# Kernel tuning notes

Hardware: AMD Instinct MI355X
Metric: run time of the kernel (lower is better)

Reference implementation:

```python
import jax, jax.numpy as jnp
import numpy as np

N_A = 100000
N_B = 100000


def _mean_agg(x_src, src, dst, n_dst):
    # gather source features along edges, mean-aggregate into destination nodes
    msgs = x_src[src]                                        # [E, d]
    s = jax.ops.segment_sum(msgs, dst, num_segments=n_dst)   # [n_dst, d]
    ones = jnp.ones((dst.shape[0], 1), dtype=x_src.dtype)
    cnt = jax.ops.segment_sum(ones, dst, num_segments=n_dst)
    return s / jnp.maximum(cnt, jnp.asarray(1.0, x_src.dtype))


def setup_inputs() -> dict:
    key = jax.random.key(0)
    ks = jax.random.split(key, 13)
    E = 1200000
    d = 64
    return {
        "x_A": jax.random.normal(ks[0], (N_A, d), jnp.float32),
        "x_B": jax.random.normal(ks[1], (N_B, d), jnp.float32),
        "Wn": jax.random.normal(ks[2], (2, 3, d, d), jnp.float32) * 0.1,
        "Wr": jax.random.normal(ks[3], (2, 3, d, d), jnp.float32) * 0.1,
        "b": jax.random.normal(ks[4], (2, 3, d), jnp.float32) * 0.1,
        "W_out": jax.random.normal(ks[5], (d, d), jnp.float32) * 0.1,
        "b_out": jax.random.normal(ks[6], (d,), jnp.float32) * 0.1,
        "src0": jax.random.randint(ks[7], (E,), 0, N_A, jnp.int64 if jax.config.jax_enable_x64 else jnp.int32),
        "dst0": jax.random.randint(ks[8], (E,), 0, N_B, jnp.int32),
        "src1": jax.random.randint(ks[9], (E,), 0, N_B, jnp.int32),
        "dst1": jax.random.randint(ks[10], (E,), 0, N_A, jnp.int32),
        "src2": jax.random.randint(ks[11], (E,), 0, N_A, jnp.int32),
        "dst2": jax.random.randint(ks[12], (E,), 0, N_A, jnp.int32),
    }


def reference(x_A, x_B, Wn, Wr, b, W_out, b_out,
              src0, dst0, src1, dst1, src2, dst2):
    # Two stacked heterogeneous conv layers (SAGEConv-style per edge type,
    # summed across edge types per destination node type), then Linear+ReLU head.
    for l in range(2):
        m0 = _mean_agg(x_A, src0, dst0, N_B)  # A -> B
        m1 = _mean_agg(x_B, src1, dst1, N_A)  # B -> A
        m2 = _mean_agg(x_A, src2, dst2, N_A)  # A -> A
        new_B = m0 @ Wn[l, 0] + x_B @ Wr[l, 0] + b[l, 0]
        new_A = (m1 @ Wn[l, 1] + x_A @ Wr[l, 1] + b[l, 1]
                 + m2 @ Wn[l, 2] + x_A @ Wr[l, 2] + b[l, 2])
        x_A, x_B = new_A, new_B
    out_A = jax.nn.relu(x_A @ W_out + b_out)
    out_B = jax.nn.relu(x_B @ W_out + b_out)
    return jnp.concatenate([out_A, out_B], axis=0)  # [N_A + N_B, d]
```

## Files before the change

### kernel.cpp

```cpp
#include <hip/hip_runtime.h>
#include <hip/hip_bf16.h>

typedef __bf16 bf16_t;
typedef unsigned short u16;
typedef short short8 __attribute__((ext_vector_type(8)));
typedef float f32x4 __attribute__((ext_vector_type(4)));

#define BSHIFT 9
#define CAP 8192
#define PTILE 8192

__device__ inline short f2bs(float v) {
    bf16_t h = (bf16_t)v;
    return __builtin_bit_cast(short, h);
}
__device__ inline float uif(unsigned u) { return __builtin_bit_cast(float, u); }

__global__ __launch_bounds__(1024, 8) void mega_prep_partition(
    const float* __restrict__ xA, const float* __restrict__ xB,
    const float* __restrict__ Wn, const float* __restrict__ Wr,
    const float* __restrict__ Wout, const float* __restrict__ b,
    const float* __restrict__ b_out,
    const int* __restrict__ s0, const int* __restrict__ d0,
    const int* __restrict__ s1, const int* __restrict__ d1,
    const int* __restrict__ s2, const int* __restrict__ d2,
    u16* __restrict__ plane0, u16* __restrict__ wh,
    int* __restrict__ gcursor, float* __restrict__ biasC,
    int* __restrict__ pairs,
    int NA, int NB, int E, int total, int ntiles) {
    __shared__ __align__(16) char smem[32768];
    int bi = blockIdx.x;
    int tid = threadIdx.x;

    if (bi < ntiles) {
        int* hist = (int*)smem;
        int* gbase = hist + 1024;
        hist[tid] = 0;
        __syncthreads();
        int tile = bi * PTILE;
        int mybkt[8], mypk[8], myrank[8];
#pragma unroll
        for (int j = 0; j < 8; j++) {
            int idx = tile + j * 1024 + tid;
            int g = -1, s = 0;
            if (idx < total) {
                if (idx < E) { s = s0[idx]; g = d0[idx]; }
                else if (idx < 2 * E) { s = s1[idx - E]; g = NB + d1[idx - E]; }
                else { s = s2[idx - 2 * E]; g = NB + NA + d2[idx - 2 * E]; }
            }
            if (g >= 0) {
                mybkt[j] = g >> BSHIFT;
                mypk[j] = ((g & ((1 << BSHIFT) - 1)) << 17) | s;
                myrank[j] = atomicAdd(&hist[mybkt[j]], 1);
            } else mybkt[j] = -1;
        }
        __syncthreads();
        {
            int c = hist[tid];
            if (c) gbase[tid] = tid * CAP + atomicAdd(&gcursor[tid], c);
        }
        __syncthreads();
#pragma unroll
        for (int j = 0; j < 8; j++) {
            if (mybkt[j] >= 0)
                pairs[gbase[mybkt[j]] + myrank[j]] = mypk[j];
        }
        return;
    }

    bi -= ntiles;
    int nA4 = NA * 16, nB4 = NB * 16;
    int bA = (nA4 + 1023) / 1024, bB = (nB4 + 1023) / 1024;
    if (bi < bA + bB) {
        const float* in = (bi < bA) ? xA : xB;
        u16* out = (bi < bA) ? plane0 : plane0 + (size_t)NA * 64;
        int i = (bi < bA ? bi : bi - bA) * 1024 + tid;
        int n4 = (bi < bA) ? nA4 : nB4;
        if (i >= n4) return;
        float4 v = ((const float4*)in)[i];
        u16 o[4];
        o[0] = (u16)f2bs(v.x); o[1] = (u16)f2bs(v.y);
        o[2] = (u16)f2bs(v.z); o[3] = (u16)f2bs(v.w);
        *(uint2*)(out + (size_t)i * 4) = *(uint2*)o;
        return;
    }
    if (bi < bA + bB + 11) {
        int mat = bi - bA - bB;
        u16* dstp = wh + (size_t)mat * 4096;
        for (int i = tid; i < 4096; i += 1024) {
            int k = i >> 6, n = i & 63;
            float v;
            if (mat < 6) v = Wn[(size_t)mat * 4096 + i];
            else if (mat < 8) v = Wr[(size_t)((mat - 6) * 3 + 0) * 4096 + i];
            else if (mat < 10) v = Wr[(size_t)((mat - 8) * 3 + 1) * 4096 + i]
                                 + Wr[(size_t)((mat - 8) * 3 + 2) * 4096 + i];
            else v = Wout[i];
            dstp[n * 64 + k] = (u16)f2bs(v);
        }
        return;
    }
    if (bi < bA + bB + 11 + 5) {
        int c = bi - bA - bB - 11;
        const float* Wsrc;
        const float* Wsrc2 = nullptr;
        if (c == 0) Wsrc = Wn + (size_t)3 * 4096;
        else if (c == 1) Wsrc = Wr + (size_t)3 * 4096;
        else if (c == 2) Wsrc = Wn + (size_t)4 * 4096;
        else if (c == 3) Wsrc = Wn + (size_t)5 * 4096;
        else { Wsrc = Wr + (size_t)4 * 4096; Wsrc2 = Wr + (size_t)5 * 4096; }
        float* Ws = (float*)smem;
        float* Wo = Ws + 4096;
        for (int i = tid; i < 4096; i += 1024) {
            float w = Wsrc[i];
            if (Wsrc2) w += Wsrc2[i];
            Ws[i] = w;
            Wo[i] = Wout[i];
        }
        __syncthreads();
        u16* dstp = wh + (size_t)(11 + c) * 4096;
        for (int it = 0; it < 4; ++it) {
            int i = it * 1024 + tid;
            int k = i >> 6, n = i & 63;
            float p0 = 0.f, p1 = 0.f, p2 = 0.f, p3 = 0.f;
#pragma unroll
            for (int j = 0; j < 64; j += 4) {
                p0 += Ws[k * 64 + j]     * Wo[j * 64 + n];
                p1 += Ws[k * 64 + j + 1] * Wo[(j + 1) * 64 + n];
                p2 += Ws[k * 64 + j + 2] * Wo[(j + 2) * 64 + n];
                p3 += Ws[k * 64 + j + 3] * Wo[(j + 3) * 64 + n];
            }
            dstp[n * 64 + k] = (u16)f2bs((p0 + p1) + (p2 + p3));
        }
        return;
    }
    if (tid < 64) {
        int n = tid;
        float s0v = b_out[n], s1v = b_out[n];
        for (int j = 0; j < 64; j++) {
            float wo = Wout[j * 64 + n];
            s0v += b[3 * 64 + j] * wo;
            s1v += (b[4 * 64 + j] + b[5 * 64 + j]) * wo;
        }
        biasC[0 * 64 + n] = b[0 * 64 + n];
        biasC[1 * 64 + n] = b[1 * 64 + n] + b[2 * 64 + n];
        biasC[2 * 64 + n] = s0v;
        biasC[3 * 64 + n] = s1v;
    }
}

__global__ __launch_bounds__(512) void bucket_fill(const int* __restrict__ pairs,
                                                   const int* __restrict__ gcursor,
                                                   int* __restrict__ off_s,
                                                   int* __restrict__ off_e,
                                                   int* __restrict__ colidx, int M) {
    int b = blockIdx.x;
    int gb = b << BSHIFT;
    __shared__ int cnt[512], cur[512], wsum[8];
    int tid = threadIdx.x;
    int lane = tid & 63, w = tid >> 6;
    int p0 = b * CAP, p1 = p0 + gcursor[b];
    cnt[tid] = 0;
    __syncthreads();
    for (int e = p0 + tid; e < p1; e += 512)
        atomicAdd(&cnt[(unsigned)pairs[e] >> 17], 1);
    __syncthreads();
    int v = cnt[tid];
    int x = v;
#pragma unroll
    for (int off = 1; off < 64; off <<= 1) {
        int n = __shfl_up(x, off);
        if (lane >= off) x += n;
    }
    if (lane == 63) wsum[w] = x;
    __syncthreads();
    if (tid == 0) {
        int s = 0;
#pragma unroll
        for (int i = 0; i < 8; i++) { int t = wsum[i]; wsum[i] = s; s += t; }
    }
    __syncthreads();
    int excl = x - v + wsum[w];
    cur[tid] = excl;
    int g = gb + tid;
    if (g < M) { off_s[g] = p0 + excl; off_e[g] = p0 + excl + v; }
    __syncthreads();
    for (int e = p0 + tid; e < p1; e += 512) {
        int p = pairs[e];
        int pos = atomicAdd(&cur[(unsigned)p >> 17], 1);
        colidx[p0 + pos] = p & 0x1FFFF;
    }
}

__device__ __forceinline__ void acc8(uint4 u, f32x4& a0, f32x4& a1) {
    a0[0] += uif(u.x << 16); a0[1] += uif(u.x & 0xFFFF0000u);
    a0[2] += uif(u.y << 16); a0[3] += uif(u.y & 0xFFFF0000u);
    a1[0] += uif(u.z << 16); a1[1] += uif(u.z & 0xFFFF0000u);
    a1[2] += uif(u.w << 16); a1[3] += uif(u.w & 0xFFFF0000u);
}

__device__ __forceinline__ uint4 gather_seg(const char* __restrict__ tab,
                                            const int* __restrict__ colidx,
                                            int s0, int s1, unsigned fo) {
    f32x4 a0 = {0.f, 0.f, 0.f, 0.f}, a1 = {0.f, 0.f, 0.f, 0.f};
    int e = s0;
    if (e + 3 < s1) {
        int c0 = colidx[e], c1 = colidx[e + 1];
        int c2 = colidx[e + 2], c3 = colidx[e + 3];
        while (e + 7 < s1) {
            uint4 u0 = *(const uint4*)(tab + (((unsigned)c0 << 7) | fo));
            uint4 u1 = *(const uint4*)(tab + (((unsigned)c1 << 7) | fo));
            uint4 u2 = *(const uint4*)(tab + (((unsigned)c2 << 7) | fo));
            uint4 u3 = *(const uint4*)(tab + (((unsigned)c3 << 7) | fo));
            c0 = colidx[e + 4]; c1 = colidx[e + 5];
            c2 = colidx[e + 6]; c3 = colidx[e + 7];
            acc8(u0, a0, a1); acc8(u1, a0, a1);
            acc8(u2, a0, a1); acc8(u3, a0, a1);
            e += 4;
        }
        {
            uint4 u0 = *(const uint4*)(tab + (((unsigned)c0 << 7) | fo));
            uint4 u1 = *(const uint4*)(tab + (((unsigned)c1 << 7) | fo));
            uint4 u2 = *(const uint4*)(tab + (((unsigned)c2 << 7) | fo));
            uint4 u3 = *(const uint4*)(tab + (((unsigned)c3 << 7) | fo));
            acc8(u0, a0, a1); acc8(u1, a0, a1);
            acc8(u2, a0, a1); acc8(u3, a0, a1);
            e += 4;
        }
    }
    for (; e < s1; ++e) {
        int c = colidx[e];
        uint4 u = *(const uint4*)(tab + (((unsigned)c << 7) | fo));
        acc8(u, a0, a1);
    }
    float inv = 1.0f / fmaxf((float)(s1 - s0), 1.0f);
    u16 o[8];
#pragma unroll
    for (int i = 0; i < 4; i++) o[i] = (u16)f2bs(a0[i] * inv);
#pragma unroll
    for (int i = 0; i < 4; i++) o[4 + i] = (u16)f2bs(a1[i] * inv);
    return *(uint4*)o;
}

template <int L2>
__global__ __launch_bounds__(256) void fused_layer(
    const u16* __restrict__ plane_in, void* __restrict__ outv,
    const int* __restrict__ colidx,
    const int* __restrict__ off_s, const int* __restrict__ off_e,
    const u16* __restrict__ wh, const float* __restrict__ biasC,
    int NA, int NB, int blocksBf) {
    __shared__ __align__(16) u16 mS[32][72];
    const int tid = threadIdx.x;
    const int w = tid >> 6, lane = tid & 63;
    const int oct = lane >> 3, fl = lane & 7;
    const unsigned fo = (unsigned)(fl << 4);
    const char* pA = (const char*)plane_in;
    const char* pB = (const char*)(plane_in + (size_t)NA * 64);
    const int r = lane & 15, q = lane >> 4;
    short8 zf;
#pragma unroll
    for (int j = 0; j < 8; j++) zf[j] = 0;

    if ((int)blockIdx.x < blocksBf) {
        const int row0 = blockIdx.x * 32;
        const int rt = w >> 1;
        const int tbase = (w & 1) * 2;
        const int arow = row0 + rt * 16 + r;
        const bool av = arow < NB;
        short8 ax0 = av ? *(const short8*)(pB + (size_t)arow * 128 + q * 16) : zf;
        short8 ax1 = av ? *(const short8*)(pB + (size_t)arow * 128 + 64 + q * 16) : zf;
        {
            int seg = w * 8 + oct;
            int brow = row0 + seg;
            int s0 = 0, s1 = 0;
            if (brow < NB) { s0 = off_s[brow]; s1 = off_e[brow]; }
            uint4 mv = gather_seg(pA, colidx, s0, s1, fo);
            *(uint4*)&mS[seg][fl * 8] = mv;
        }
        __syncthreads();
        const u16* WmT = wh + (size_t)(L2 ? 11 : 0) * 4096;
        const u16* WxT = wh + (size_t)(L2 ? 12 : 6) * 4096;
        const float* bb = biasC + (size_t)(L2 ? 2 : 0) * 64;
        f32x4 acc[2];
#pragma unroll
        for (int t2 = 0; t2 < 2; t2++) {
            float bv = bb[(tbase + t2) * 16 + r];
            acc[t2][0] = bv; acc[t2][1] = bv; acc[t2][2] = bv; acc[t2][3] = bv;
        }
#pragma unroll
        for (int ks = 0; ks < 2; ks++) {
            short8 am = *(const short8*)&mS[rt * 16 + r][ks * 32 + q * 8];
            short8 ax = ks ? ax1 : ax0;
#pragma unroll
            for (int t2 = 0; t2 < 2; t2++) {
                size_t widx = (size_t)((tbase + t2) * 16 + r) * 64 + ks * 32 + q * 8;
                acc[t2] = __builtin_amdgcn_mfma_f32_16x16x32_bf16(am, *(const short8*)(WmT + widx), acc[t2], 0, 0, 0);
                acc[t2] = __builtin_amdgcn_mfma_f32_16x16x32_bf16(ax, *(const short8*)(WxT + widx), acc[t2], 0, 0, 0);
            }
        }
#pragma unroll
        for (int t2 = 0; t2 < 2; t2++) {
            int col = (tbase + t2) * 16 + r;
#pragma unroll
            for (int rr = 0; rr < 4; rr++) {
                int row = row0 + rt * 16 + q * 4 + rr;
                if (row < NB) {
                    float v = acc[t2][rr];
                    if (L2) __builtin_nontemporal_store(fmaxf(v, 0.0f),
                                (float*)outv + (size_t)(NA + row) * 64 + col);
                    else ((u16*)outv)[(size_t)(NA + row) * 64 + col] = (u16)f2bs(v);
                }
            }
        }
    } else {
        const int row0 = ((int)blockIdx.x - blocksBf) * 16;
        const int t = w;
        const int arow = row0 + r;
        const bool av = arow < NA;
        short8 ax0 = av ? *(const short8*)(pA + (size_t)arow * 128 + q * 16) : zf;
        short8 ax1 = av ? *(const short8*)(pA + (size_t)arow * 128 + 64 + q * 16) : zf;
        {
            int seg = w * 8 + oct;
            int rrow = row0 + (seg & 15);
            bool m2 = seg >= 16;
            int s0 = 0, s1 = 0;
            if (rrow < NA) {
                int g = m2 ? (NB + NA + rrow) : (NB + rrow);
                s0 = off_s[g]; s1 = off_e[g];
            }
            uint4 mv = gather_seg(m2 ? pA : pB, colidx, s0, s1, fo);
            *(uint4*)&mS[seg][fl * 8] = mv;
        }
        __syncthreads();
        const u16* Wm1T = wh + (size_t)(L2 ? 13 : 1) * 4096;
        const u16* Wm2T = wh + (size_t)(L2 ? 14 : 2) * 4096;
        const u16* WxT  = wh + (size_t)(L2 ? 15 : 8) * 4096;
        const float* bb = biasC + (size_t)(L2 ? 3 : 1) * 64;
        f32x4 acc;
        {
            float bv = bb[t * 16 + r];
            acc[0] = bv; acc[1] = bv; acc[2] = bv; acc[3] = bv;
        }
#pragma unroll
        for (int ks = 0; ks < 2; ks++) {
            short8 am1 = *(const short8*)&mS[r][ks * 32 + q * 8];
            short8 am2 = *(const short8*)&mS[16 + r][ks * 32 + q * 8];
            short8 ax = ks ? ax1 : ax0;
            size_t widx = (size_t)(t * 16 + r) * 64 + ks * 32 + q * 8;
            acc = __builtin_amdgcn_mfma_f32_16x16x32_bf16(am1, *(const short8*)(Wm1T + widx), acc, 0, 0, 0);
            acc = __builtin_amdgcn_mfma_f32_16x16x32_bf16(am2, *(const short8*)(Wm2T + widx), acc, 0, 0, 0);
            acc = __builtin_amdgcn_mfma_f32_16x16x32_bf16(ax, *(const short8*)(WxT + widx), acc, 0, 0, 0);
        }
        {
            int col = t * 16 + r;
#pragma unroll
            for (int rr = 0; rr < 4; rr++) {
                int row = row0 + q * 4 + rr;
                if (row < NA) {
                    float v = acc[rr];
                    if (L2) __builtin_nontemporal_store(fmaxf(v, 0.0f),
                                (float*)outv + (size_t)row * 64 + col);
                    else ((u16*)outv)[(size_t)row * 64 + col] = (u16)f2bs(v);
                }
            }
        }
    }
}

extern "C" void kernel_launch(void* const* d_in, const int* in_sizes, int n_in,
                              void* d_out, int out_size, void* d_ws, size_t ws_size,
                              hipStream_t stream) {
    const float* xA_in = (const float*)d_in[0];
    const float* xB_in = (const float*)d_in[1];
    const float* Wn = (const float*)d_in[2];
    const float* Wr = (const float*)d_in[3];
    const float* b = (const float*)d_in[4];
    const float* W_out = (const float*)d_in[5];
    const float* b_out = (const float*)d_in[6];
    const int* src0 = (const int*)d_in[7];
    const int* dst0 = (const int*)d_in[8];
    const int* src1 = (const int*)d_in[9];
    const int* dst1 = (const int*)d_in[10];
    const int* src2 = (const int*)d_in[11];
    const int* dst2 = (const int*)d_in[12];

    const int NA = in_sizes[0] / 64;
    const int NB = in_sizes[1] / 64;
    const int E = in_sizes[7];
    const int M = NB + NA + NA;
    const int total = 3 * E;
    const int K = (M + (1 << BSHIFT) - 1) >> BSHIFT;

    const size_t PL = (size_t)(NA + NB) * 64;
    u16* plane[2];
    plane[0] = (u16*)d_ws;
    plane[1] = plane[0] + PL;
    u16* wh     = plane[1] + PL;
    int* gcursor= (int*)(wh + 16 * 4096);
    float* biasC= (float*)(gcursor + 1024);
    int* off_s  = (int*)(biasC + 256);
    int* off_e  = off_s + M;
    int* colidx = off_e + M;
    int* pairs  = colidx + (size_t)K * CAP;

    int bA = (NA * 16 + 1023) / 1024, bB = (NB * 16 + 1023) / 1024;
    int ntiles = (total + PTILE - 1) / PTILE;
    hipMemsetAsync(gcursor, 0, 1024 * 4, stream);
    mega_prep_partition<<<ntiles + bA + bB + 11 + 5 + 1, 1024, 0, stream>>>(
        xA_in, xB_in, Wn, Wr, W_out, b, b_out,
        src0, dst0, src1, dst1, src2, dst2,
        plane[0], wh, gcursor, biasC, pairs, NA, NB, E, total, ntiles);

    bucket_fill<<<K, 512, 0, stream>>>(pairs, gcursor, off_s, off_e, colidx, M);

    const int blocksBf = (NB + 31) / 32;
    const int blocksAf = (NA + 15) / 16;
    fused_layer<0><<<blocksBf + blocksAf, 256, 0, stream>>>(
        plane[0], plane[1], colidx, off_s, off_e, wh, biasC, NA, NB, blocksBf);
    fused_layer<1><<<blocksBf + blocksAf, 256, 0, stream>>>(
        plane[1], d_out, colidx, off_s, off_e, wh, biasC, NA, NB, blocksBf);
}
```

Before: 359.8 us.

## Make each wave own a full 16-row tile in fused layer kernels

Reorganizes fused_layer so each 64-lane wave handles an entire 16-row tile on its own: it gathers all segments for its rows into a private LDS slice and computes all four 16-column output tiles with MFMA. Blocks shrink to 128 threads (two independent waves), and the block-wide __syncthreads is replaced by a wave barrier. The aim is to remove cross-wave synchronization stalls, where uneven gather lengths made every wave wait for the slowest one, and to let waves progress independently. In exchange each wave does serial gathers over twice as many segments (two passes per lane), holds more accumulators in registers, and reloads the weights per wave.

```diff
diff --git a/kernel.cpp b/kernel.cpp
--- a/kernel.cpp
+++ b/kernel.cpp
@@ -242,69 +242,72 @@
 }
 
 template <int L2>
-__global__ __launch_bounds__(256) void fused_layer(
+__global__ __launch_bounds__(128) void fused_layer(
     const u16* __restrict__ plane_in, void* __restrict__ outv,
     const int* __restrict__ colidx,
     const int* __restrict__ off_s, const int* __restrict__ off_e,
     const u16* __restrict__ wh, const float* __restrict__ biasC,
-    int NA, int NB, int blocksBf) {
-    __shared__ __align__(16) u16 mS[32][72];
+    int NA, int NB, int tileB) {
+    __shared__ __align__(16) u16 mS[2][2][16][72];
     const int tid = threadIdx.x;
     const int w = tid >> 6, lane = tid & 63;
     const int oct = lane >> 3, fl = lane & 7;
     const unsigned fo = (unsigned)(fl << 4);
+    const int r = lane & 15, q = lane >> 4;
+    const int tileA = (NA + 15) / 16;
+    const int wv = (int)blockIdx.x * 2 + w;
+    if (wv >= tileB + tileA) return;
     const char* pA = (const char*)plane_in;
     const char* pB = (const char*)(plane_in + (size_t)NA * 64);
-    const int r = lane & 15, q = lane >> 4;
+    u16 (* __restrict__ mT0)[72] = mS[w][0];
+    u16 (* __restrict__ mT1)[72] = mS[w][1];
     short8 zf;
 #pragma unroll
     for (int j = 0; j < 8; j++) zf[j] = 0;
 
-    if ((int)blockIdx.x < blocksBf) {
-        const int row0 = blockIdx.x * 32;
-        const int rt = w >> 1;
-        const int tbase = (w & 1) * 2;
-        const int arow = row0 + rt * 16 + r;
+    if (wv < tileB) {
+        const int row0 = wv * 16;
+        const int arow = row0 + r;
         const bool av = arow < NB;
         short8 ax0 = av ? *(const short8*)(pB + (size_t)arow * 128 + q * 16) : zf;
         short8 ax1 = av ? *(const short8*)(pB + (size_t)arow * 128 + 64 + q * 16) : zf;
-        {
-            int seg = w * 8 + oct;
-            int brow = row0 + seg;
+#pragma unroll
+        for (int s = 0; s < 2; s++) {
+            int row = row0 + oct + s * 8;
             int s0 = 0, s1 = 0;
-            if (brow < NB) { s0 = off_s[brow]; s1 = off_e[brow]; }
+            if (row < NB) { s0 = off_s[row]; s1 = off_e[row]; }
             uint4 mv = gather_seg(pA, colidx, s0, s1, fo);
-            *(uint4*)&mS[seg][fl * 8] = mv;
-        }
-        __syncthreads();
+            *(uint4*)&mT0[oct + s * 8][fl * 8] = mv;
+        }
+        __builtin_amdgcn_wave_barrier();
         const u16* WmT = wh + (size_t)(L2 ? 11 : 0) * 4096;
         const u16* WxT = wh + (size_t)(L2 ? 12 : 6) * 4096;
         const float* bb = biasC + (size_t)(L2 ? 2 : 0) * 64;
-        f32x4 acc[2];
-#pragma unroll
-        for (int t2 = 0; t2 < 2; t2++) {
-            float bv = bb[(tbase + t2) * 16 + r];
-            acc[t2][0] = bv; acc[t2][1] = bv; acc[t2][2] = bv; acc[t2][3] = bv;
+        f32x4 acc[4];
+#pragma unroll
+        for (int t = 0; t < 4; t++) {
+            float bv = bb[t * 16 + r];
+            acc[t][0] = bv; acc[t][1] = bv; acc[t][2] = bv; acc[t][3] = bv;
         }
 #pragma unroll
         for (int ks = 0; ks < 2; ks++) {
-            short8 am = *(const short8*)&mS[rt * 16 + r][ks * 32 + q * 8];
+            short8 am = *(const short8*)&mT0[r][ks * 32 + q * 8];
             short8 ax = ks ? ax1 : ax0;
 #pragma unroll
-            for (int t2 = 0; t2 < 2; t2++) {
-                size_t widx = (size_t)((tbase + t2) * 16 + r) * 64 + ks * 32 + q * 8;
-                acc[t2] = __builtin_amdgcn_mfma_f32_16x16x32_bf16(am, *(const short8*)(WmT + widx), acc[t2], 0, 0, 0);
-                acc[t2] = __builtin_amdgcn_mfma_f32_16x16x32_bf16(ax, *(const short8*)(WxT + widx), acc[t2], 0, 0, 0);
-            }
-        }
-#pragma unroll
-        for (int t2 = 0; t2 < 2; t2++) {
-            int col = (tbase + t2) * 16 + r;
+            for (int t = 0; t < 4; t++) {
+                size_t widx = (size_t)(t * 16 + r) * 64 + ks * 32 + q * 8;
+                acc[t] = __builtin_amdgcn_mfma_f32_16x16x32_bf16(am, *(const short8*)(WmT + widx), acc[t], 0, 0, 0);
+                acc[t] = __builtin_amdgcn_mfma_f32_16x16x32_bf16(ax, *(const short8*)(WxT + widx), acc[t], 0, 0, 0);
+            }
+        }
+#pragma unroll
+        for (int t = 0; t < 4; t++) {
+            int col = t * 16 + r;
 #pragma unroll
             for (int rr = 0; rr < 4; rr++) {
-                int row = row0 + rt * 16 + q * 4 + rr;
+                int row = row0 + q * 4 + rr;
                 if (row < NB) {
-                    float v = acc[t2][rr];
+                    float v = acc[t][rr];
                     if (L2) __builtin_nontemporal_store(fmaxf(v, 0.0f),
                                 (float*)outv + (size_t)(NA + row) * 64 + col);
                     else ((u16*)outv)[(size_t)(NA + row) * 64 + col] = (u16)f2bs(v);
@@ -312,51 +315,57 @@
             }
         }
     } else {
-        const int row0 = ((int)blockIdx.x - blocksBf) * 16;
-        const int t = w;
+        const int row0 = (wv - tileB) * 16;
         const int arow = row0 + r;
         const bool av = arow < NA;
         short8 ax0 = av ? *(const short8*)(pA + (size_t)arow * 128 + q * 16) : zf;
         short8 ax1 = av ? *(const short8*)(pA + (size_t)arow * 128 + 64 + q * 16) : zf;
-        {
-            int seg = w * 8 + oct;
-            int rrow = row0 + (seg & 15);
-            bool m2 = seg >= 16;
-            int s0 = 0, s1 = 0;
-            if (rrow < NA) {
-                int g = m2 ? (NB + NA + rrow) : (NB + rrow);
-                s0 = off_s[g]; s1 = off_e[g];
-            }
-            uint4 mv = gather_seg(m2 ? pA : pB, colidx, s0, s1, fo);
-            *(uint4*)&mS[seg][fl * 8] = mv;
-        }
-        __syncthreads();
+#pragma unroll
+        for (int s = 0; s < 2; s++) {
+            int row = row0 + oct + s * 8;
+            int a0 = 0, a1 = 0, b0 = 0, b1 = 0;
+            if (row < NA) {
+                int g1 = NB + row, g2 = NB + NA + row;
+                a0 = off_s[g1]; a1 = off_e[g1];
+                b0 = off_s[g2]; b1 = off_e[g2];
+            }
+            uint4 v1 = gather_seg(pB, colidx, a0, a1, fo);
+            *(uint4*)&mT0[oct + s * 8][fl * 8] = v1;
+            uint4 v2 = gather_seg(pA, colidx, b0, b1, fo);
+            *(uint4*)&mT1[oct + s * 8][fl * 8] = v2;
+        }
+        __builtin_amdgcn_wave_barrier();
         const u16* Wm1T = wh + (size_t)(L2 ? 13 : 1) * 4096;
         const u16* Wm2T = wh + (size_t)(L2 ? 14 : 2) * 4096;
         const u16* WxT  = wh + (size_t)(L2 ? 15 : 8) * 4096;
         const float* bb = biasC + (size_t)(L2 ? 3 : 1) * 64;
-        f32x4 acc;
-        {
+        f32x4 acc[4];
+#pragma unroll
+        for (int t = 0; t < 4; t++) {
             float bv = bb[t * 16 + r];
-            acc[0] = bv; acc[1] = bv; acc[2] = bv; acc[3] = bv;
+            acc[t][0] = bv; acc[t][1] = bv; acc[t][2] = bv; acc[t][3] = bv;
         }
 #pragma unroll
         for (int ks = 0; ks < 2; ks++) {
-            short8 am1 = *(const short8*)&mS[r][ks * 32 + q * 8];
-            short8 am2 = *(const short8*)&mS[16 + r][ks * 32 + q * 8];
+            short8 am1 = *(const short8*)&mT0[r][ks * 32 + q * 8];
+            short8 am2 = *(const short8*)&mT1[r][ks * 32 + q * 8];
             short8 ax = ks ? ax1 : ax0;
-            size_t widx = (size_t)(t * 16 + r) * 64 + ks * 32 + q * 8;
-            acc = __builtin_amdgcn_mfma_f32_16x16x32_bf16(am1, *(const short8*)(Wm1T + widx), acc, 0, 0, 0);
-            acc = __builtin_amdgcn_mfma_f32_16x16x32_bf16(am2, *(const short8*)(Wm2T + widx), acc, 0, 0, 0);
-            acc = __builtin_amdgcn_mfma_f32_16x16x32_bf16(ax, *(const short8*)(WxT + widx), acc, 0, 0, 0);
-        }
-        {
+#pragma unroll
+            for (int t = 0; t < 4; t++) {
+                size_t widx = (size_t)(t * 16 + r) * 64 + ks * 32 + q * 8;
+                acc[t] = __builtin_amdgcn_mfma_f32_16x16x32_bf16(am1, *(const short8*)(Wm1T + widx), acc[t], 0, 0, 0);
+                acc[t] = __builtin_amdgcn_mfma_f32_16x16x32_bf16(am2, *(const short8*)(Wm2T + widx), acc[t], 0, 0, 0);
+                acc[t] = __builtin_amdgcn_mfma_f32_16x16x32_bf16(ax, *(const short8*)(WxT + widx), acc[t], 0, 0, 0);
+            }
+        }
+#pragma unroll
+        for (int t = 0; t < 4; t++) {
             int col = t * 16 + r;
 #pragma unroll
             for (int rr = 0; rr < 4; rr++) {
                 int row = row0 + q * 4 + rr;
                 if (row < NA) {
-                    float v = acc[rr];
+                    float v = acc[t][rr];
                     if (L2) __builtin_nontemporal_store(fmaxf(v, 0.0f),
                                 (float*)outv + (size_t)row * 64 + col);
                     else ((u16*)outv)[(size_t)row * 64 + col] = (u16)f2bs(v);
@@ -412,10 +421,11 @@
 
     bucket_fill<<<K, 512, 0, stream>>>(pairs, gcursor, off_s, off_e, colidx, M);
 
-    const int blocksBf = (NB + 31) / 32;
-    const int blocksAf = (NA + 15) / 16;
-    fused_layer<0><<<blocksBf + blocksAf, 256, 0, stream>>>(
-        plane[0], plane[1], colidx, off_s, off_e, wh, biasC, NA, NB, blocksBf);
-    fused_layer<1><<<blocksBf + blocksAf, 256, 0, stream>>>(
-        plane[1], d_out, colidx, off_s, off_e, wh, biasC, NA, NB, blocksBf);
-}
+    const int tileB = (NB + 15) / 16;
+    const int tileA = (NA + 15) / 16;
+    const int nblk = (tileB + tileA + 1) / 2;
+    fused_layer<0><<<nblk, 128, 0, stream>>>(
+        plane[0], plane[1], colidx, off_s, off_e, wh, biasC, NA, NB, tileB);
+    fused_layer<1><<<nblk, 128, 0, stream>>>(
+        plane[1], d_out, colidx, off_s, off_e, wh, biasC, NA, NB, tileB);
+}
```

Result: slower. 370.9 us (+3.1%).

## Gather two segments per 8-lane group and double rows per block

Applied to the files above, without the earlier changes.

Each 8-lane group now interleaves the gathers for two destination segments (two B rows, or the m1 and m2 segments of one A row), which keeps more independent loads in flight per thread. Block tiles double to 64 B rows and 32 A rows, so each block computes more output tiles per weight load and the grid has half as many blocks. The cost is higher register use for the dual accumulators, predicated loads in the unified loop, and fewer blocks for load balancing across skewed degrees.

```diff
diff --git a/kernel.cpp b/kernel.cpp
--- a/kernel.cpp
+++ b/kernel.cpp
@@ -198,47 +198,39 @@
     a1[2] += uif(u.w << 16); a1[3] += uif(u.w & 0xFFFF0000u);
 }
 
-__device__ __forceinline__ uint4 gather_seg(const char* __restrict__ tab,
-                                            const int* __restrict__ colidx,
-                                            int s0, int s1, unsigned fo) {
-    f32x4 a0 = {0.f, 0.f, 0.f, 0.f}, a1 = {0.f, 0.f, 0.f, 0.f};
-    int e = s0;
-    if (e + 3 < s1) {
-        int c0 = colidx[e], c1 = colidx[e + 1];
-        int c2 = colidx[e + 2], c3 = colidx[e + 3];
-        while (e + 7 < s1) {
-            uint4 u0 = *(const uint4*)(tab + (((unsigned)c0 << 7) | fo));
-            uint4 u1 = *(const uint4*)(tab + (((unsigned)c1 << 7) | fo));
-            uint4 u2 = *(const uint4*)(tab + (((unsigned)c2 << 7) | fo));
-            uint4 u3 = *(const uint4*)(tab + (((unsigned)c3 << 7) | fo));
-            c0 = colidx[e + 4]; c1 = colidx[e + 5];
-            c2 = colidx[e + 6]; c3 = colidx[e + 7];
-            acc8(u0, a0, a1); acc8(u1, a0, a1);
-            acc8(u2, a0, a1); acc8(u3, a0, a1);
-            e += 4;
-        }
-        {
-            uint4 u0 = *(const uint4*)(tab + (((unsigned)c0 << 7) | fo));
-            uint4 u1 = *(const uint4*)(tab + (((unsigned)c1 << 7) | fo));
-            uint4 u2 = *(const uint4*)(tab + (((unsigned)c2 << 7) | fo));
-            uint4 u3 = *(const uint4*)(tab + (((unsigned)c3 << 7) | fo));
-            acc8(u0, a0, a1); acc8(u1, a0, a1);
-            acc8(u2, a0, a1); acc8(u3, a0, a1);
-            e += 4;
-        }
-    }
-    for (; e < s1; ++e) {
-        int c = colidx[e];
-        uint4 u = *(const uint4*)(tab + (((unsigned)c << 7) | fo));
-        acc8(u, a0, a1);
-    }
-    float inv = 1.0f / fmaxf((float)(s1 - s0), 1.0f);
-    u16 o[8];
-#pragma unroll
-    for (int i = 0; i < 4; i++) o[i] = (u16)f2bs(a0[i] * inv);
-#pragma unroll
-    for (int i = 0; i < 4; i++) o[4 + i] = (u16)f2bs(a1[i] * inv);
-    return *(uint4*)o;
+__device__ __forceinline__ void gather2(const char* __restrict__ ta, int a0, int a1,
+                                        const char* __restrict__ tb, int b0, int b1,
+                                        const int* __restrict__ colidx, unsigned fo,
+                                        u16* __restrict__ outA, u16* __restrict__ outB) {
+    f32x4 pa0 = {0.f,0.f,0.f,0.f}, pa1 = {0.f,0.f,0.f,0.f};
+    f32x4 qb0 = {0.f,0.f,0.f,0.f}, qb1 = {0.f,0.f,0.f,0.f};
+    int e1 = a0, e2 = b0;
+    while (e1 < a1 || e2 < b1) {
+        int n1 = a1 - e1; n1 = n1 > 4 ? 4 : n1;
+        int n2 = b1 - e2; n2 = n2 > 4 ? 4 : n2;
+        uint4 r1[4], r2[4];
+#pragma unroll
+        for (int j = 0; j < 4; j++)
+            if (j < n1) { int c = colidx[e1 + j]; r1[j] = *(const uint4*)(ta + (((unsigned)c << 7) | fo)); }
+#pragma unroll
+        for (int j = 0; j < 4; j++)
+            if (j < n2) { int c = colidx[e2 + j]; r2[j] = *(const uint4*)(tb + (((unsigned)c << 7) | fo)); }
+#pragma unroll
+        for (int j = 0; j < 4; j++) if (j < n1) acc8(r1[j], pa0, pa1);
+#pragma unroll
+        for (int j = 0; j < 4; j++) if (j < n2) acc8(r2[j], qb0, qb1);
+        e1 += n1; e2 += n2;
+    }
+    float inva = 1.0f / fmaxf((float)(a1 - a0), 1.0f);
+    float invb = 1.0f / fmaxf((float)(b1 - b0), 1.0f);
+    u16 oa[8], ob[8];
+#pragma unroll
+    for (int i = 0; i < 4; i++) {
+        oa[i] = (u16)f2bs(pa0[i] * inva); oa[4 + i] = (u16)f2bs(pa1[i] * inva);
+        ob[i] = (u16)f2bs(qb0[i] * invb); ob[4 + i] = (u16)f2bs(qb1[i] * invb);
+    }
+    *(uint4*)outA = *(uint4*)oa;
+    *(uint4*)outB = *(uint4*)ob;
 }
 
 template <int L2>
@@ -248,7 +240,7 @@
     const int* __restrict__ off_s, const int* __restrict__ off_e,
     const u16* __restrict__ wh, const float* __restrict__ biasC,
     int NA, int NB, int blocksBf) {
-    __shared__ __align__(16) u16 mS[32][72];
+    __shared__ __align__(16) u16 mS[64][72];
     const int tid = threadIdx.x;
     const int w = tid >> 6, lane = tid & 63;
     const int oct = lane >> 3, fl = lane & 7;
@@ -256,55 +248,54 @@
     const char* pA = (const char*)plane_in;
     const char* pB = (const char*)(plane_in + (size_t)NA * 64);
     const int r = lane & 15, q = lane >> 4;
+    const int seg = w * 8 + oct;
     short8 zf;
 #pragma unroll
     for (int j = 0; j < 8; j++) zf[j] = 0;
 
     if ((int)blockIdx.x < blocksBf) {
-        const int row0 = blockIdx.x * 32;
-        const int rt = w >> 1;
-        const int tbase = (w & 1) * 2;
-        const int arow = row0 + rt * 16 + r;
+        const int row0 = blockIdx.x * 64;
+        const int arow = row0 + w * 16 + r;
         const bool av = arow < NB;
         short8 ax0 = av ? *(const short8*)(pB + (size_t)arow * 128 + q * 16) : zf;
         short8 ax1 = av ? *(const short8*)(pB + (size_t)arow * 128 + 64 + q * 16) : zf;
         {
-            int seg = w * 8 + oct;
-            int brow = row0 + seg;
-            int s0 = 0, s1 = 0;
-            if (brow < NB) { s0 = off_s[brow]; s1 = off_e[brow]; }
-            uint4 mv = gather_seg(pA, colidx, s0, s1, fo);
-            *(uint4*)&mS[seg][fl * 8] = mv;
+            int ra = row0 + seg, rb = row0 + seg + 32;
+            int a0 = 0, a1 = 0, b0 = 0, b1 = 0;
+            if (ra < NB) { a0 = off_s[ra]; a1 = off_e[ra]; }
+            if (rb < NB) { b0 = off_s[rb]; b1 = off_e[rb]; }
+            gather2(pA, a0, a1, pA, b0, b1, colidx, fo,
+                    &mS[seg][fl * 8], &mS[seg + 32][fl * 8]);
         }
         __syncthreads();
         const u16* WmT = wh + (size_t)(L2 ? 11 : 0) * 4096;
         const u16* WxT = wh + (size_t)(L2 ? 12 : 6) * 4096;
         const float* bb = biasC + (size_t)(L2 ? 2 : 0) * 64;
-        f32x4 acc[2];
-#pragma unroll
-        for (int t2 = 0; t2 < 2; t2++) {
-            float bv = bb[(tbase + t2) * 16 + r];
-            acc[t2][0] = bv; acc[t2][1] = bv; acc[t2][2] = bv; acc[t2][3] = bv;
+        f32x4 acc[4];
+#pragma unroll
+        for (int t = 0; t < 4; t++) {
+            float bv = bb[t * 16 + r];
+            acc[t][0] = bv; acc[t][1] = bv; acc[t][2] = bv; acc[t][3] = bv;
         }
 #pragma unroll
         for (int ks = 0; ks < 2; ks++) {
-            short8 am = *(const short8*)&mS[rt * 16 + r][ks * 32 + q * 8];
+            short8 am = *(const short8*)&mS[w * 16 + r][ks * 32 + q * 8];
             short8 ax = ks ? ax1 : ax0;
 #pragma unroll
-            for (int t2 = 0; t2 < 2; t2++) {
-                size_t widx = (size_t)((tbase + t2) * 16 + r) * 64 + ks * 32 + q * 8;
-                acc[t2] = __builtin_amdgcn_mfma_f32_16x16x32_bf16(am, *(const short8*)(WmT + widx), acc[t2], 0, 0, 0);
-                acc[t2] = __builtin_amdgcn_mfma_f32_16x16x32_bf16(ax, *(const short8*)(WxT + widx), acc[t2], 0, 0, 0);
-            }
-        }
-#pragma unroll
-        for (int t2 = 0; t2 < 2; t2++) {
-            int col = (tbase + t2) * 16 + r;
+            for (int t = 0; t < 4; t++) {
+                size_t widx = (size_t)(t * 16 + r) * 64 + ks * 32 + q * 8;
+                acc[t] = __builtin_amdgcn_mfma_f32_16x16x32_bf16(am, *(const short8*)(WmT + widx), acc[t], 0, 0, 0);
+                acc[t] = __builtin_amdgcn_mfma_f32_16x16x32_bf16(ax, *(const short8*)(WxT + widx), acc[t], 0, 0, 0);
+            }
+        }
+#pragma unroll
+        for (int t = 0; t < 4; t++) {
+            int col = t * 16 + r;
 #pragma unroll
             for (int rr = 0; rr < 4; rr++) {
-                int row = row0 + rt * 16 + q * 4 + rr;
+                int row = row0 + w * 16 + q * 4 + rr;
                 if (row < NB) {
-                    float v = acc[t2][rr];
+                    float v = acc[t][rr];
                     if (L2) __builtin_nontemporal_store(fmaxf(v, 0.0f),
                                 (float*)outv + (size_t)(NA + row) * 64 + col);
                     else ((u16*)outv)[(size_t)(NA + row) * 64 + col] = (u16)f2bs(v);
@@ -312,51 +303,56 @@
             }
         }
     } else {
-        const int row0 = ((int)blockIdx.x - blocksBf) * 16;
-        const int t = w;
-        const int arow = row0 + r;
+        const int row0 = ((int)blockIdx.x - blocksBf) * 32;
+        const int rt = w >> 1;
+        const int tbase = (w & 1) * 2;
+        const int arow = row0 + rt * 16 + r;
         const bool av = arow < NA;
         short8 ax0 = av ? *(const short8*)(pA + (size_t)arow * 128 + q * 16) : zf;
         short8 ax1 = av ? *(const short8*)(pA + (size_t)arow * 128 + 64 + q * 16) : zf;
         {
-            int seg = w * 8 + oct;
-            int rrow = row0 + (seg & 15);
-            bool m2 = seg >= 16;
-            int s0 = 0, s1 = 0;
-            if (rrow < NA) {
-                int g = m2 ? (NB + NA + rrow) : (NB + rrow);
-                s0 = off_s[g]; s1 = off_e[g];
-            }
-            uint4 mv = gather_seg(m2 ? pA : pB, colidx, s0, s1, fo);
-            *(uint4*)&mS[seg][fl * 8] = mv;
+            int row = row0 + seg;
+            int a0 = 0, a1 = 0, b0 = 0, b1 = 0;
+            if (row < NA) {
+                int g1 = NB + row, g2 = NB + NA + row;
+                a0 = off_s[g1]; a1 = off_e[g1];
+                b0 = off_s[g2]; b1 = off_e[g2];
+            }
+            gather2(pB, a0, a1, pA, b0, b1, colidx, fo,
+                    &mS[seg][fl * 8], &mS[seg + 32][fl * 8]);
         }
         __syncthreads();
         const u16* Wm1T = wh + (size_t)(L2 ? 13 : 1) * 4096;
         const u16* Wm2T = wh + (size_t)(L2 ? 14 : 2) * 4096;
         const u16* WxT  = wh + (size_t)(L2 ? 15 : 8) * 4096;
         const float* bb = biasC + (size_t)(L2 ? 3 : 1) * 64;
-        f32x4 acc;
-        {
-            float bv = bb[t * 16 + r];
-            acc[0] = bv; acc[1] = bv; acc[2] = bv; acc[3] = bv;
+        f32x4 acc[2];
+#pragma unroll
+        for (int t2 = 0; t2 < 2; t2++) {
+            float bv = bb[(tbase + t2) * 16 + r];
+            acc[t2][0] = bv; acc[t2][1] = bv; acc[t2][2] = bv; acc[t2][3] = bv;
         }
 #pragma unroll
         for (int ks = 0; ks < 2; ks++) {
-            short8 am1 = *(const short8*)&mS[r][ks * 32 + q * 8];
-            short8 am2 = *(const short8*)&mS[16 + r][ks * 32 + q * 8];
+            short8 am1 = *(const short8*)&mS[rt * 16 + r][ks * 32 + q * 8];
+            short8 am2 = *(const short8*)&mS[32 + rt * 16 + r][ks * 32 + q * 8];
             short8 ax = ks ? ax1 : ax0;
-            size_t widx = (size_t)(t * 16 + r) * 64 + ks * 32 + q * 8;
-            acc = __builtin_amdgcn_mfma_f32_16x16x32_bf16(am1, *(const short8*)(Wm1T + widx), acc, 0, 0, 0);
-            acc = __builtin_amdgcn_mfma_f32_16x16x32_bf16(am2, *(const short8*)(Wm2T + widx), acc, 0, 0, 0);
-            acc = __builtin_amdgcn_mfma_f32_16x16x32_bf16(ax, *(const short8*)(WxT + widx), acc, 0, 0, 0);
-        }
-        {
-            int col = t * 16 + r;
+#pragma unroll
+            for (int t2 = 0; t2 < 2; t2++) {
+                size_t widx = (size_t)((tbase + t2) * 16 + r) * 64 + ks * 32 + q * 8;
+                acc[t2] = __builtin_amdgcn_mfma_f32_16x16x32_bf16(am1, *(const short8*)(Wm1T + widx), acc[t2], 0, 0, 0);
+                acc[t2] = __builtin_amdgcn_mfma_f32_16x16x32_bf16(am2, *(const short8*)(Wm2T + widx), acc[t2], 0, 0, 0);
+                acc[t2] = __builtin_amdgcn_mfma_f32_16x16x32_bf16(ax, *(const short8*)(WxT + widx), acc[t2], 0, 0, 0);
+            }
+        }
+#pragma unroll
+        for (int t2 = 0; t2 < 2; t2++) {
+            int col = (tbase + t2) * 16 + r;
 #pragma unroll
             for (int rr = 0; rr < 4; rr++) {
-                int row = row0 + q * 4 + rr;
+                int row = row0 + rt * 16 + q * 4 + rr;
                 if (row < NA) {
-                    float v = acc[rr];
+                    float v = acc[t2][rr];
                     if (L2) __builtin_nontemporal_store(fmaxf(v, 0.0f),
                                 (float*)outv + (size_t)row * 64 + col);
                     else ((u16*)outv)[(size_t)row * 64 + col] = (u16)f2bs(v);
@@ -412,8 +408,8 @@
 
     bucket_fill<<<K, 512, 0, stream>>>(pairs, gcursor, off_s, off_e, colidx, M);
 
-    const int blocksBf = (NB + 31) / 32;
-    const int blocksAf = (NA + 15) / 16;
+    const int blocksBf = (NB + 63) / 64;
+    const int blocksAf = (NA + 31) / 32;
     fused_layer<0><<<blocksBf + blocksAf, 256, 0, stream>>>(
         plane[0], plane[1], colidx, off_s, off_e, wh, biasC, NA, NB, blocksBf);
     fused_layer<1><<<blocksBf + blocksAf, 256, 0, stream>>>(
```

After: 442.2 us. +22.9%, slower.

## Sort destination rows by degree to balance gather work per block

Applied to the files above, without the earlier changes.

Adds a degree histogram kernel and a counting-sort scatter kernel that build per-node-type row permutations grouped by in-degree (capped at 127). Both fused layers then process rows in permuted order, indirecting the input feature load, segment offsets and output writes through the permutation. The intent is to cut load imbalance and lane divergence in the per-segment gather loops, since each 8-lane group waits on the longest segment in its block. In exchange it adds two small kernel launches and an extra indirection, and output stores and self-feature loads become scattered rather than contiguous.

```diff
diff --git a/kernel.cpp b/kernel.cpp
--- a/kernel.cpp
+++ b/kernel.cpp
@@ -188,6 +188,88 @@
         int p = pairs[e];
         int pos = atomicAdd(&cur[(unsigned)p >> 17], 1);
         colidx[p0 + pos] = p & 0x1FFFF;
+    }
+}
+
+__global__ __launch_bounds__(256) void deg_hist(const int* __restrict__ off_s,
+                                                const int* __restrict__ off_e,
+                                                int* __restrict__ binsB,
+                                                int* __restrict__ binsA,
+                                                int NA, int NB) {
+    __shared__ int hB[128], hA[128];
+    int tid = threadIdx.x;
+    if (tid < 128) { hB[tid] = 0; hA[tid] = 0; }
+    __syncthreads();
+    int totalR = NB + NA;
+    for (int i = blockIdx.x * 256 + tid; i < totalR; i += gridDim.x * 256) {
+        if (i < NB) {
+            int d = off_e[i] - off_s[i];
+            atomicAdd(&hB[d > 127 ? 127 : d], 1);
+        } else {
+            int row = i - NB;
+            int d1 = off_e[NB + row] - off_s[NB + row];
+            int d2 = off_e[NB + NA + row] - off_s[NB + NA + row];
+            int d = d1 > d2 ? d1 : d2;
+            atomicAdd(&hA[d > 127 ? 127 : d], 1);
+        }
+    }
+    __syncthreads();
+    if (tid < 128) {
+        if (hB[tid]) atomicAdd(&binsB[tid], hB[tid]);
+        if (hA[tid]) atomicAdd(&binsA[tid], hA[tid]);
+    }
+}
+
+__global__ __launch_bounds__(1024) void perm_scatter(const int* __restrict__ off_s,
+                                                     const int* __restrict__ off_e,
+                                                     const int* __restrict__ binsB,
+                                                     const int* __restrict__ binsA,
+                                                     int* __restrict__ bcurB,
+                                                     int* __restrict__ bcurA,
+                                                     int* __restrict__ rowpermB,
+                                                     int* __restrict__ rowpermA,
+                                                     int NA, int NB) {
+    __shared__ int lhB[128], lhA[128], lbB[128], lbA[128], pB[128], pA[128];
+    int tid = threadIdx.x;
+    if (tid < 128) { lhB[tid] = 0; lhA[tid] = 0; }
+    __syncthreads();
+    int i = blockIdx.x * 1024 + tid;
+    int bin = -1, rank = 0, isB = 0, row = 0;
+    if (i < NB + NA) {
+        if (i < NB) {
+            row = i;
+            int d = off_e[i] - off_s[i];
+            bin = d > 127 ? 127 : d; isB = 1;
+            rank = atomicAdd(&lhB[bin], 1);
+        } else {
+            row = i - NB;
+            int d1 = off_e[NB + row] - off_s[NB + row];
+            int d2 = off_e[NB + NA + row] - off_s[NB + NA + row];
+            int d = d1 > d2 ? d1 : d2;
+            bin = d > 127 ? 127 : d;
+            rank = atomicAdd(&lhA[bin], 1);
+        }
+    }
+    __syncthreads();
+    if (tid == 0) {
+        int s = 0;
+        for (int k = 0; k < 128; k++) { pB[k] = s; s += binsB[k]; }
+        s = 0;
+        for (int k = 0; k < 128; k++) { pA[k] = s; s += binsA[k]; }
+    }
+    __syncthreads();
+    if (tid < 128) {
+        int c = lhB[tid];
+        if (c) lbB[tid] = pB[tid] + atomicAdd(&bcurB[tid], c);
+    } else if (tid < 256) {
+        int t = tid - 128;
+        int c = lhA[t];
+        if (c) lbA[t] = pA[t] + atomicAdd(&bcurA[t], c);
+    }
+    __syncthreads();
+    if (bin >= 0) {
+        if (isB) rowpermB[lbB[bin] + rank] = row;
+        else     rowpermA[lbA[bin] + rank] = row;
     }
 }
 
@@ -246,6 +328,7 @@
     const u16* __restrict__ plane_in, void* __restrict__ outv,
     const int* __restrict__ colidx,
     const int* __restrict__ off_s, const int* __restrict__ off_e,
+    const int* __restrict__ rowpermB, const int* __restrict__ rowpermA,
     const u16* __restrict__ wh, const float* __restrict__ biasC,
     int NA, int NB, int blocksBf) {
     __shared__ __align__(16) u16 mS[32][72];
@@ -264,15 +347,16 @@
         const int row0 = blockIdx.x * 32;
         const int rt = w >> 1;
         const int tbase = (w & 1) * 2;
-        const int arow = row0 + rt * 16 + r;
-        const bool av = arow < NB;
+        const int aidx = row0 + rt * 16 + r;
+        const bool av = aidx < NB;
+        const int arow = av ? rowpermB[aidx] : 0;
         short8 ax0 = av ? *(const short8*)(pB + (size_t)arow * 128 + q * 16) : zf;
         short8 ax1 = av ? *(const short8*)(pB + (size_t)arow * 128 + 64 + q * 16) : zf;
         {
             int seg = w * 8 + oct;
-            int brow = row0 + seg;
+            int idx = row0 + seg;
             int s0 = 0, s1 = 0;
-            if (brow < NB) { s0 = off_s[brow]; s1 = off_e[brow]; }
+            if (idx < NB) { int brow = rowpermB[idx]; s0 = off_s[brow]; s1 = off_e[brow]; }
             uint4 mv = gather_seg(pA, colidx, s0, s1, fo);
             *(uint4*)&mS[seg][fl * 8] = mv;
         }
@@ -302,29 +386,32 @@
             int col = (tbase + t2) * 16 + r;
 #pragma unroll
             for (int rr = 0; rr < 4; rr++) {
-                int row = row0 + rt * 16 + q * 4 + rr;
-                if (row < NB) {
+                int oidx = row0 + rt * 16 + q * 4 + rr;
+                if (oidx < NB) {
+                    int orow = rowpermB[oidx];
                     float v = acc[t2][rr];
                     if (L2) __builtin_nontemporal_store(fmaxf(v, 0.0f),
-                                (float*)outv + (size_t)(NA + row) * 64 + col);
-                    else ((u16*)outv)[(size_t)(NA + row) * 64 + col] = (u16)f2bs(v);
+                                (float*)outv + (size_t)(NA + orow) * 64 + col);
+                    else ((u16*)outv)[(size_t)(NA + orow) * 64 + col] = (u16)f2bs(v);
                 }
             }
         }
     } else {
         const int row0 = ((int)blockIdx.x - blocksBf) * 16;
         const int t = w;
-        const int arow = row0 + r;
-        const bool av = arow < NA;
+        const int aidx = row0 + r;
+        const bool av = aidx < NA;
+        const int arow = av ? rowpermA[aidx] : 0;
         short8 ax0 = av ? *(const short8*)(pA + (size_t)arow * 128 + q * 16) : zf;
         short8 ax1 = av ? *(const short8*)(pA + (size_t)arow * 128 + 64 + q * 16) : zf;
         {
             int seg = w * 8 + oct;
-            int rrow = row0 + (seg & 15);
+            int idx = row0 + (seg & 15);
             bool m2 = seg >= 16;
             int s0 = 0, s1 = 0;
-            if (rrow < NA) {
-                int g = m2 ? (NB + NA + rrow) : (NB + rrow);
+            if (idx < NA) {
+                int prow = rowpermA[idx];
+                int g = m2 ? (NB + NA + prow) : (NB + prow);
                 s0 = off_s[g]; s1 = off_e[g];
             }
             uint4 mv = gather_seg(m2 ? pA : pB, colidx, s0, s1, fo);
@@ -354,12 +441,13 @@
             int col = t * 16 + r;
 #pragma unroll
             for (int rr = 0; rr < 4; rr++) {
-                int row = row0 + q * 4 + rr;
-                if (row < NA) {
+                int oidx = row0 + q * 4 + rr;
+                if (oidx < NA) {
+                    int orow = rowpermA[oidx];
                     float v = acc[rr];
                     if (L2) __builtin_nontemporal_store(fmaxf(v, 0.0f),
-                                (float*)outv + (size_t)row * 64 + col);
-                    else ((u16*)outv)[(size_t)row * 64 + col] = (u16)f2bs(v);
+                                (float*)outv + (size_t)orow * 64 + col);
+                    else ((u16*)outv)[(size_t)orow * 64 + col] = (u16)f2bs(v);
                 }
             }
         }
@@ -394,17 +482,23 @@
     u16* plane[2];
     plane[0] = (u16*)d_ws;
     plane[1] = plane[0] + PL;
-    u16* wh     = plane[1] + PL;
-    int* gcursor= (int*)(wh + 16 * 4096);
-    float* biasC= (float*)(gcursor + 1024);
-    int* off_s  = (int*)(biasC + 256);
-    int* off_e  = off_s + M;
-    int* colidx = off_e + M;
-    int* pairs  = colidx + (size_t)K * CAP;
+    u16* wh      = plane[1] + PL;
+    int* gcursor = (int*)(wh + 16 * 4096);
+    int* binsB   = gcursor + 1024;
+    int* binsA   = binsB + 128;
+    int* bcurB   = binsA + 128;
+    int* bcurA   = bcurB + 128;
+    float* biasC = (float*)(bcurA + 128);
+    int* off_s   = (int*)(biasC + 256);
+    int* off_e   = off_s + M;
+    int* rowpermB= off_e + M;
+    int* rowpermA= rowpermB + NB;
+    int* colidx  = rowpermA + NA;
+    int* pairs   = colidx + (size_t)K * CAP;
 
     int bA = (NA * 16 + 1023) / 1024, bB = (NB * 16 + 1023) / 1024;
     int ntiles = (total + PTILE - 1) / PTILE;
-    hipMemsetAsync(gcursor, 0, 1024 * 4, stream);
+    hipMemsetAsync(gcursor, 0, (1024 + 512) * 4, stream);
     mega_prep_partition<<<ntiles + bA + bB + 11 + 5 + 1, 1024, 0, stream>>>(
         xA_in, xB_in, Wn, Wr, W_out, b, b_out,
         src0, dst0, src1, dst1, src2, dst2,
@@ -412,10 +506,16 @@
 
     bucket_fill<<<K, 512, 0, stream>>>(pairs, gcursor, off_s, off_e, colidx, M);
 
+    deg_hist<<<512, 256, 0, stream>>>(off_s, off_e, binsB, binsA, NA, NB);
+    perm_scatter<<<(NB + NA + 1023) / 1024, 1024, 0, stream>>>(
+        off_s, off_e, binsB, binsA, bcurB, bcurA, rowpermB, rowpermA, NA, NB);
+
     const int blocksBf = (NB + 31) / 32;
     const int blocksAf = (NA + 15) / 16;
     fused_layer<0><<<blocksBf + blocksAf, 256, 0, stream>>>(
-        plane[0], plane[1], colidx, off_s, off_e, wh, biasC, NA, NB, blocksBf);
+        plane[0], plane[1], colidx, off_s, off_e, rowpermB, rowpermA,
+        wh, biasC, NA, NB, blocksBf);
     fused_layer<1><<<blocksBf + blocksAf, 256, 0, stream>>>(
-        plane[1], d_out, colidx, off_s, off_e, wh, biasC, NA, NB, blocksBf);
-}
+        plane[1], d_out, colidx, off_s, off_e, rowpermB, rowpermA,
+        wh, biasC, NA, NB, blocksBf);
+}
```

Result: slower. 377.8 us (+5.0%).
